# Kernel tuning notes

Measured on AMD Instinct MI355X. Metric: run time of the kernel, lower is better.

## Reference

```python
import jax, jax.numpy as jnp
import numpy as np

OUT_H, OUT_W = 64, 64  # glimpse size (layer's output_dim)
B, IMG_H, IMG_W, CH = 32, 512, 512, 3


def setup_inputs() -> dict:
    key = jax.random.key(0)
    k_img, k_u, k_s, k_d, k_u2, k_s2, k_d2 = jax.random.split(key, 7)
    img_tensor = jax.random.uniform(k_img, (B, IMG_H, IMG_W, CH), dtype=jnp.float32)
    # DRAW-style params per sample: (uy, sy, dy, ux, sx, dx)
    # centres u in [0, img - glimpse], sigma s in [1, 5], stride d in [1, img/glimpse]
    uy = jax.random.uniform(k_u, (B, 1), minval=0.0, maxval=IMG_H - OUT_H * 2.0)
    sy = jax.random.uniform(k_s, (B, 1), minval=1.0, maxval=5.0)
    dy = jax.random.uniform(k_d, (B, 1), minval=1.0, maxval=IMG_H / OUT_H)
    ux = jax.random.uniform(k_u2, (B, 1), minval=0.0, maxval=IMG_W - OUT_W * 2.0)
    sx = jax.random.uniform(k_s2, (B, 1), minval=1.0, maxval=5.0)
    dx = jax.random.uniform(k_d2, (B, 1), minval=1.0, maxval=IMG_W / OUT_W)
    transform_params = jnp.concatenate([uy, sy, dy, ux, sx, dx], axis=-1)  # (B, 6)
    return {"img_tensor": img_tensor, "transform_params": transform_params}


def gaussian_mask(u, s, d, R, C):
    """Normalized Gaussian filterbank.
    u, s, d: (B, 1) centre of first Gaussian, std, stride between centres.
    R: number of glimpse rows/cols; C: image size along that axis.
    Returns (B, C, R), each column normalized to sum 1 (plus eps)."""
    r = jnp.arange(R, dtype=jnp.float32).reshape(1, 1, R)
    c = jnp.arange(C, dtype=jnp.float32).reshape(1, C, 1)
    centres = u[:, None, :] + r * d[:, None, :]            # (B, 1, R)
    mask = jnp.exp(-0.5 * jnp.square((c - centres) / s[:, None, :]))  # (B, C, R)
    return mask / (jnp.sum(mask, axis=1, keepdims=True) + 1e-8)


def reference(img_tensor, transform_params):
    # img_tensor: (B, h, w, ch); transform_params: (B, 6)
    _, h, w, _ = img_tensor.shape
    uy, sy, dy, ux, sx, dx = jnp.split(transform_params, 6, axis=-1)
    Ay = gaussian_mask(uy, sy, dy, OUT_H, h)  # (B, h, OUT_H)
    Ax = gaussian_mask(ux, sx, dx, OUT_W, w)  # (B, w, OUT_W)
    # glimpse = Ay^T @ img @ Ax, applied per channel
    g = jnp.einsum('bhH,bhwc->bHwc', Ay, img_tensor)   # (B, OUT_H, w, ch)
    return jnp.einsum('bHwc,bwW->bHWc', g, Ax)         # (B, OUT_H, OUT_W, ch)
```

## Files before the change

kernel.cpp:

```cpp
#include <hip/hip_runtime.h>

#define BATCH 32
#define IMG 512
#define CH 3
#define GOUT 64
#define ROWB (IMG*CH)

typedef __attribute__((ext_vector_type(8))) short  short8;
typedef __attribute__((ext_vector_type(4))) float  floatx4;

__device__ __forceinline__ unsigned short f2bf(float x) {
    unsigned u = __builtin_bit_cast(unsigned, x);
    u += 0x7FFFu + ((u >> 16) & 1u);
    return (unsigned short)(u >> 16);
}

__global__ __launch_bounds__(64) void mask_kernel(const float* __restrict__ tp,
                                                  unsigned short* __restrict__ AyT,
                                                  unsigned short* __restrict__ AxT) {
    int blk  = blockIdx.x;
    int r    = blk & 63;
    int axis = (blk >> 6) & 1;
    int b    = blk >> 7;

    const float* p = tp + b*6 + (axis ? 3 : 0);
    float u = p[0], s = p[1], d = p[2];
    float centre = u + (float)r * d;
    float inv_s  = 1.0f / s;

    int lane = threadIdx.x;
    float e[8];
    float sum = 0.0f;
    #pragma unroll
    for (int i = 0; i < 8; ++i) {
        float z = ((float)(i*64 + lane) - centre) * inv_s;
        e[i] = __expf(-0.5f * z * z);
        sum += e[i];
    }
    #pragma unroll
    for (int m = 1; m < 64; m <<= 1)
        sum += __shfl_xor(sum, m, 64);
    float inv_sum = 1.0f / (sum + 1e-8f);

    unsigned short* dst = (axis ? AxT : AyT) + ((size_t)b*GOUT + r) * IMG;
    #pragma unroll
    for (int i = 0; i < 8; ++i)
        dst[i*64 + lane] = f2bf(e[i] * inv_sum);
}

__global__ __launch_bounds__(256) void stage1_kernel(const float* __restrict__ img,
                                                     const unsigned short* __restrict__ AyT,
                                                     float* __restrict__ gP) {
    int tile = blockIdx.x % 24;
    int b    = blockIdx.x / 24;
    int tid  = threadIdx.x;
    int wave = tid >> 6;
    int lane = tid & 63;
    int n16  = lane & 15;
    int q    = lane >> 4;
    int wc   = tile*64 + wave*16 + n16;

    floatx4 acc[4];
    #pragma unroll
    for (int mt = 0; mt < 4; ++mt) acc[mt] = (floatx4){0.f, 0.f, 0.f, 0.f};

    const unsigned short* ayb = AyT + ((size_t)b*GOUT + n16) * IMG;

    for (int h0 = 0; h0 < IMG; h0 += 32) {
        const float* bp = img + ((size_t)(b*IMG + h0 + q*8)) * ROWB + wc;
        short8 bf;
        #pragma unroll
        for (int j = 0; j < 8; ++j)
            bf[j] = (short)f2bf(bp[(size_t)j * ROWB]);

        #pragma unroll
        for (int mt = 0; mt < 4; ++mt) {
            short8 af = *(const short8*)(ayb + (size_t)mt*16*IMG + h0 + q*8);
            acc[mt] = __builtin_amdgcn_mfma_f32_16x16x32_bf16(af, bf, acc[mt], 0, 0, 0);
        }
    }

    int c = wc % 3, w = wc / 3;
    float* gb = gP + ((size_t)(b*CH + c) * GOUT) * IMG + w;
    #pragma unroll
    for (int mt = 0; mt < 4; ++mt) {
        int Hbase = mt*16 + q*4;
        #pragma unroll
        for (int reg = 0; reg < 4; ++reg)
            gb[(size_t)(Hbase + reg) * IMG] = acc[mt][reg];
    }
}

__global__ __launch_bounds__(256) void stage2_kernel(const float* __restrict__ gP,
                                                     const unsigned short* __restrict__ AxT,
                                                     float* __restrict__ out) {
    int blk  = blockIdx.x;
    int part = blk & 3;
    int bc   = blk >> 2;
    int c    = bc % 3;
    int b    = bc / 3;
    int tid  = threadIdx.x;
    int wm   = tid >> 6;
    int lane = tid & 63;
    int n16  = lane & 15;
    int q    = lane >> 4;

    floatx4 acc[4];
    #pragma unroll
    for (int nt = 0; nt < 4; ++nt) acc[nt] = (floatx4){0.f, 0.f, 0.f, 0.f};

    const float*          ga  = gP  + ((size_t)(b*CH + c) * GOUT + wm*16 + n16) * IMG;
    const unsigned short* axb = AxT + ((size_t)b*GOUT + n16) * IMG;

    #pragma unroll
    for (int cc = 0; cc < 4; ++cc) {
        int w0 = part*128 + cc*32;
        const float* ap = ga + w0 + q*8;
        short8 af;
        #pragma unroll
        for (int j = 0; j < 8; ++j)
            af[j] = (short)f2bf(ap[j]);

        #pragma unroll
        for (int nt = 0; nt < 4; ++nt) {
            short8 bf = *(const short8*)(axb + (size_t)nt*16*IMG + w0 + q*8);
            acc[nt] = __builtin_amdgcn_mfma_f32_16x16x32_bf16(af, bf, acc[nt], 0, 0, 0);
        }
    }

    #pragma unroll
    for (int nt = 0; nt < 4; ++nt) {
        int W = nt*16 + n16;
        #pragma unroll
        for (int reg = 0; reg < 4; ++reg) {
            int H = wm*16 + q*4 + reg;
            atomicAdd(out + (((size_t)b*GOUT + H) * GOUT + W) * CH + c, acc[nt][reg]);
        }
    }
}

extern "C" void kernel_launch(void* const* d_in, const int* in_sizes, int n_in,
                              void* d_out, int out_size, void* d_ws, size_t ws_size,
                              hipStream_t stream) {
    const float* img = (const float*)d_in[0];
    const float* tp  = (const float*)d_in[1];
    float* out = (float*)d_out;

    unsigned short* AyT = (unsigned short*)d_ws;
    unsigned short* AxT = AyT + (size_t)BATCH * GOUT * IMG;
    float*          gP  = (float*)(AxT + (size_t)BATCH * GOUT * IMG);

    hipMemsetAsync(d_out, 0, (size_t)out_size * sizeof(float), stream);
    mask_kernel  <<<BATCH * 2 * GOUT,  64, 0, stream>>>(tp, AyT, AxT);
    stage1_kernel<<<BATCH * 24,       256, 0, stream>>>(img, AyT, gP);
    stage2_kernel<<<BATCH * CH * 4,   256, 0, stream>>>(gP, AxT, out);
}
```

Measured before the change: 190.1 us.

## Stage image and mask tiles through LDS with vectorized loads in stage1

Stage1 now loads 64-row by 128-column image tiles and the matching Ay mask slice into shared memory using float4/uint4 loads, then feeds MFMAs from LDS. Each wave computes two N-tiles, and the grid is halved to 12 tiles per batch. The goal is to replace the strided scalar global loads with coalesced ones, at the cost of barriers, LDS footprint and fewer blocks. Stage2 also switches its A-fragment load to two float4 loads.

```diff
diff --git a/kernel.cpp b/kernel.cpp
--- a/kernel.cpp
+++ b/kernel.cpp
@@ -51,43 +51,78 @@
 __global__ __launch_bounds__(256) void stage1_kernel(const float* __restrict__ img,
                                                      const unsigned short* __restrict__ AyT,
                                                      float* __restrict__ gP) {
-    int tile = blockIdx.x % 24;
-    int b    = blockIdx.x / 24;
+    __shared__ float          Bs[64][132];
+    __shared__ unsigned short As[64][72];
+
+    int tile = blockIdx.x % 12;
+    int b    = blockIdx.x / 12;
+    int wc0  = tile * 128;
     int tid  = threadIdx.x;
     int wave = tid >> 6;
     int lane = tid & 63;
     int n16  = lane & 15;
     int q    = lane >> 4;
-    int wc   = tile*64 + wave*16 + n16;
 
-    floatx4 acc[4];
+    floatx4 acc[4][2];
     #pragma unroll
-    for (int mt = 0; mt < 4; ++mt) acc[mt] = (floatx4){0.f, 0.f, 0.f, 0.f};
+    for (int mt = 0; mt < 4; ++mt)
+        #pragma unroll
+        for (int nt = 0; nt < 2; ++nt)
+            acc[mt][nt] = (floatx4){0.f, 0.f, 0.f, 0.f};
 
-    const unsigned short* ayb = AyT + ((size_t)b*GOUT + n16) * IMG;
+    const float*          imb = img + (size_t)b * IMG * ROWB + wc0;
+    const unsigned short* ayb = AyT + (size_t)b * GOUT * IMG;
 
-    for (int h0 = 0; h0 < IMG; h0 += 32) {
-        const float* bp = img + ((size_t)(b*IMG + h0 + q*8)) * ROWB + wc;
-        short8 bf;
+    for (int h0 = 0; h0 < IMG; h0 += 64) {
         #pragma unroll
-        for (int j = 0; j < 8; ++j)
-            bf[j] = (short)f2bf(bp[(size_t)j * ROWB]);
+        for (int i = 0; i < 8; ++i) {
+            int p  = tid + i*256;
+            int r  = p >> 5;
+            int cg = p & 31;
+            float4 v = *(const float4*)(imb + (size_t)(h0 + r) * ROWB + cg*4);
+            *(float4*)&Bs[r][cg*4] = v;
+        }
+        #pragma unroll
+        for (int i = 0; i < 2; ++i) {
+            int p    = tid + i*256;
+            int r    = p >> 3;
+            int koff = (p & 7) * 8;
+            uint4 v = *(const uint4*)(ayb + (size_t)r * IMG + h0 + koff);
+            *(uint4*)&As[r][koff] = v;
+        }
+        __syncthreads();
 
         #pragma unroll
-        for (int mt = 0; mt < 4; ++mt) {
-            short8 af = *(const short8*)(ayb + (size_t)mt*16*IMG + h0 + q*8);
-            acc[mt] = __builtin_amdgcn_mfma_f32_16x16x32_bf16(af, bf, acc[mt], 0, 0, 0);
+        for (int s = 0; s < 2; ++s) {
+            short8 af[4];
+            #pragma unroll
+            for (int mt = 0; mt < 4; ++mt)
+                af[mt] = *(const short8*)&As[mt*16 + n16][s*32 + q*8];
+            #pragma unroll
+            for (int nt = 0; nt < 2; ++nt) {
+                short8 bf;
+                #pragma unroll
+                for (int j = 0; j < 8; ++j)
+                    bf[j] = (short)f2bf(Bs[s*32 + q*8 + j][wave*32 + nt*16 + n16]);
+                #pragma unroll
+                for (int mt = 0; mt < 4; ++mt)
+                    acc[mt][nt] = __builtin_amdgcn_mfma_f32_16x16x32_bf16(
+                        af[mt], bf, acc[mt][nt], 0, 0, 0);
+            }
         }
+        __syncthreads();
     }
 
-    int c = wc % 3, w = wc / 3;
-    float* gb = gP + ((size_t)(b*CH + c) * GOUT) * IMG + w;
     #pragma unroll
-    for (int mt = 0; mt < 4; ++mt) {
-        int Hbase = mt*16 + q*4;
+    for (int nt = 0; nt < 2; ++nt) {
+        int wc = wc0 + wave*32 + nt*16 + n16;
+        int c = wc % 3, w = wc / 3;
+        float* gb = gP + ((size_t)(b*CH + c) * GOUT) * IMG + w;
         #pragma unroll
-        for (int reg = 0; reg < 4; ++reg)
-            gb[(size_t)(Hbase + reg) * IMG] = acc[mt][reg];
+        for (int mt = 0; mt < 4; ++mt)
+            #pragma unroll
+            for (int reg = 0; reg < 4; ++reg)
+                gb[(size_t)(mt*16 + q*4 + reg) * IMG] = acc[mt][nt][reg];
     }
 }
 
@@ -116,10 +151,13 @@
     for (int cc = 0; cc < 4; ++cc) {
         int w0 = part*128 + cc*32;
         const float* ap = ga + w0 + q*8;
+        float4 a0 = *(const float4*)ap;
+        float4 a1 = *(const float4*)(ap + 4);
         short8 af;
-        #pragma unroll
-        for (int j = 0; j < 8; ++j)
-            af[j] = (short)f2bf(ap[j]);
+        af[0] = (short)f2bf(a0.x); af[1] = (short)f2bf(a0.y);
+        af[2] = (short)f2bf(a0.z); af[3] = (short)f2bf(a0.w);
+        af[4] = (short)f2bf(a1.x); af[5] = (short)f2bf(a1.y);
+        af[6] = (short)f2bf(a1.z); af[7] = (short)f2bf(a1.w);
 
         #pragma unroll
         for (int nt = 0; nt < 4; ++nt) {
@@ -152,6 +190,6 @@
 
     hipMemsetAsync(d_out, 0, (size_t)out_size * sizeof(float), stream);
     mask_kernel  <<<BATCH * 2 * GOUT,  64, 0, stream>>>(tp, AyT, AxT);
-    stage1_kernel<<<BATCH * 24,       256, 0, stream>>>(img, AyT, gP);
+    stage1_kernel<<<BATCH * 12,       256, 0, stream>>>(img, AyT, gP);
     stage2_kernel<<<BATCH * CH * 4,   256, 0, stream>>>(gP, AxT, out);
 }
```

Measured after the change: 199.8 us. +5.1%, slower.

## Stage image tiles in LDS via async loads and split stage-1 reduction over height

Applied to the files above, without the earlier changes.

Stage 1 now loads 64x64 fp32 image tiles into shared memory with direct global-to-LDS async loads and stages the Ay mask tile in LDS, in place of strided per-lane scalar global reads. The height reduction is split into two halves across twice as many blocks, each writing a separate partial buffer. Stage 2 sums the two partials with vectorized float4 loads before converting to bf16. The aim is better coalescing and more parallelism in the memory-bound first stage. In exchange it doubles the intermediate buffer traffic and workspace size and adds block-level syncs.

```diff
diff --git a/kernel.cpp b/kernel.cpp
--- a/kernel.cpp
+++ b/kernel.cpp
@@ -1,10 +1,12 @@
 #include <hip/hip_runtime.h>
+#include <stdint.h>
 
 #define BATCH 32
 #define IMG 512
 #define CH 3
 #define GOUT 64
 #define ROWB (IMG*CH)
+#define GP   ((size_t)BATCH*CH*GOUT*IMG)
 
 typedef __attribute__((ext_vector_type(8))) short  short8;
 typedef __attribute__((ext_vector_type(4))) float  floatx4;
@@ -13,6 +15,13 @@
     unsigned u = __builtin_bit_cast(unsigned, x);
     u += 0x7FFFu + ((u >> 16) & 1u);
     return (unsigned short)(u >> 16);
+}
+
+typedef __attribute__((address_space(3))) unsigned int  lds_u32;
+typedef __attribute__((address_space(1))) const unsigned int g_u32;
+__device__ __forceinline__ void async16(const void* g, void* l) {
+    __builtin_amdgcn_global_load_lds((g_u32*)(uintptr_t)g,
+                                     (lds_u32*)(uintptr_t)l, 16, 0, 0);
 }
 
 __global__ __launch_bounds__(64) void mask_kernel(const float* __restrict__ tp,
@@ -48,47 +57,75 @@
         dst[i*64 + lane] = f2bf(e[i] * inv_sum);
 }
 
-__global__ __launch_bounds__(256) void stage1_kernel(const float* __restrict__ img,
-                                                     const unsigned short* __restrict__ AyT,
-                                                     float* __restrict__ gP) {
-    int tile = blockIdx.x % 24;
-    int b    = blockIdx.x / 24;
+__global__ __launch_bounds__(256, 6) void stage1_kernel(const float* __restrict__ img,
+                                                        const unsigned short* __restrict__ AyT,
+                                                        float* __restrict__ gP) {
+    __shared__ float          Bs[64][64];
+    __shared__ unsigned short As[64][72];
+
+    int part = blockIdx.x & 1;
+    int bt   = blockIdx.x >> 1;
+    int tile = bt % 24;
+    int b    = bt / 24;
+    int wc0  = tile * 64;
     int tid  = threadIdx.x;
     int wave = tid >> 6;
     int lane = tid & 63;
     int n16  = lane & 15;
     int q    = lane >> 4;
-    int wc   = tile*64 + wave*16 + n16;
 
     floatx4 acc[4];
     #pragma unroll
     for (int mt = 0; mt < 4; ++mt) acc[mt] = (floatx4){0.f, 0.f, 0.f, 0.f};
 
-    const unsigned short* ayb = AyT + ((size_t)b*GOUT + n16) * IMG;
+    const float*          imb = img + (size_t)b * IMG * ROWB + wc0;
+    const unsigned short* ayb = AyT + (size_t)b * GOUT * IMG;
 
-    for (int h0 = 0; h0 < IMG; h0 += 32) {
-        const float* bp = img + ((size_t)(b*IMG + h0 + q*8)) * ROWB + wc;
-        short8 bf;
+    int rb = (tid >> 6)*4 + ((tid & 63) >> 4);
+    int cg = tid & 15;
+
+    for (int h0 = part*256; h0 < part*256 + 256; h0 += 64) {
+        uint4 av[2];
         #pragma unroll
-        for (int j = 0; j < 8; ++j)
-            bf[j] = (short)f2bf(bp[(size_t)j * ROWB]);
+        for (int i = 0; i < 2; ++i) {
+            int p = tid + i*256;
+            av[i] = *(const uint4*)(ayb + (size_t)(p >> 3) * IMG + h0 + (p & 7)*8);
+        }
+        #pragma unroll
+        for (int i = 0; i < 4; ++i) {
+            int r = rb + i*16;
+            async16(imb + (size_t)(h0 + r) * ROWB + cg*4, &Bs[r][cg*4]);
+        }
+        #pragma unroll
+        for (int i = 0; i < 2; ++i) {
+            int p = tid + i*256;
+            *(uint4*)&As[p >> 3][(p & 7)*8] = av[i];
+        }
+        __syncthreads();
 
         #pragma unroll
-        for (int mt = 0; mt < 4; ++mt) {
-            short8 af = *(const short8*)(ayb + (size_t)mt*16*IMG + h0 + q*8);
-            acc[mt] = __builtin_amdgcn_mfma_f32_16x16x32_bf16(af, bf, acc[mt], 0, 0, 0);
+        for (int s = 0; s < 2; ++s) {
+            short8 bf;
+            #pragma unroll
+            for (int j = 0; j < 8; ++j)
+                bf[j] = (short)f2bf(Bs[s*32 + q*8 + j][wave*16 + n16]);
+            #pragma unroll
+            for (int mt = 0; mt < 4; ++mt) {
+                short8 af = *(const short8*)&As[mt*16 + n16][s*32 + q*8];
+                acc[mt] = __builtin_amdgcn_mfma_f32_16x16x32_bf16(af, bf, acc[mt], 0, 0, 0);
+            }
         }
+        __syncthreads();
     }
 
+    int wc = wc0 + wave*16 + n16;
     int c = wc % 3, w = wc / 3;
-    float* gb = gP + ((size_t)(b*CH + c) * GOUT) * IMG + w;
+    float* gb = gP + (size_t)part * GP + ((size_t)(b*CH + c) * GOUT) * IMG + w;
     #pragma unroll
-    for (int mt = 0; mt < 4; ++mt) {
-        int Hbase = mt*16 + q*4;
+    for (int mt = 0; mt < 4; ++mt)
         #pragma unroll
         for (int reg = 0; reg < 4; ++reg)
-            gb[(size_t)(Hbase + reg) * IMG] = acc[mt][reg];
-    }
+            gb[(size_t)(mt*16 + q*4 + reg) * IMG] = acc[mt][reg];
 }
 
 __global__ __launch_bounds__(256) void stage2_kernel(const float* __restrict__ gP,
@@ -116,10 +153,15 @@
     for (int cc = 0; cc < 4; ++cc) {
         int w0 = part*128 + cc*32;
         const float* ap = ga + w0 + q*8;
+        float4 a0 = *(const float4*)ap;
+        float4 a1 = *(const float4*)(ap + 4);
+        float4 b0 = *(const float4*)(ap + GP);
+        float4 b1 = *(const float4*)(ap + GP + 4);
         short8 af;
-        #pragma unroll
-        for (int j = 0; j < 8; ++j)
-            af[j] = (short)f2bf(ap[j]);
+        af[0] = (short)f2bf(a0.x + b0.x); af[1] = (short)f2bf(a0.y + b0.y);
+        af[2] = (short)f2bf(a0.z + b0.z); af[3] = (short)f2bf(a0.w + b0.w);
+        af[4] = (short)f2bf(a1.x + b1.x); af[5] = (short)f2bf(a1.y + b1.y);
+        af[6] = (short)f2bf(a1.z + b1.z); af[7] = (short)f2bf(a1.w + b1.w);
 
         #pragma unroll
         for (int nt = 0; nt < 4; ++nt) {
@@ -148,10 +190,10 @@
 
     unsigned short* AyT = (unsigned short*)d_ws;
     unsigned short* AxT = AyT + (size_t)BATCH * GOUT * IMG;
-    float*          gP  = (float*)(AxT + (size_t)BATCH * GOUT * IMG);
+    float*          gPp = (float*)(AxT + (size_t)BATCH * GOUT * IMG);
 
     hipMemsetAsync(d_out, 0, (size_t)out_size * sizeof(float), stream);
-    mask_kernel  <<<BATCH * 2 * GOUT,  64, 0, stream>>>(tp, AyT, AxT);
-    stage1_kernel<<<BATCH * 24,       256, 0, stream>>>(img, AyT, gP);
-    stage2_kernel<<<BATCH * CH * 4,   256, 0, stream>>>(gP, AxT, out);
+    mask_kernel  <<<BATCH * 2 * GOUT,   64, 0, stream>>>(tp, AyT, AxT);
+    stage1_kernel<<<BATCH * 24 * 2,    256, 0, stream>>>(img, AyT, gPp);
+    stage2_kernel<<<BATCH * CH * 4,    256, 0, stream>>>(gPp, AxT, out);
 }
```

After: 185.9 us. 2.2% less time.

## Double-buffer image tiles via async global-to-LDS loads and store intermediate as bf16

Applied to the files above, without the earlier changes.

Stage 1 now streams image rows into LDS with asynchronous global_load_lds, double-buffered, and prefetches the next Ay fragments while the current MFMAs run. Blocks shrink to 128 threads with twice as many blocks. The intermediate is written as bf16 instead of fp32, which halves the intermediate traffic and lets stage 2 load fragments with single vector loads instead of converting per element. This adds an extra bf16 rounding of the intermediate, and correctness relies on the hand-written vmcnt waits matching the number of outstanding loads.

```diff
diff --git a/kernel.cpp b/kernel.cpp
--- a/kernel.cpp
+++ b/kernel.cpp
@@ -1,4 +1,5 @@
 #include <hip/hip_runtime.h>
+#include <stdint.h>
 
 #define BATCH 32
 #define IMG 512
@@ -13,6 +14,13 @@
     unsigned u = __builtin_bit_cast(unsigned, x);
     u += 0x7FFFu + ((u >> 16) & 1u);
     return (unsigned short)(u >> 16);
+}
+
+typedef __attribute__((address_space(3))) unsigned int  lds_u32;
+typedef __attribute__((address_space(1))) const unsigned int g_u32;
+__device__ __forceinline__ void async16(const void* g, void* l) {
+    __builtin_amdgcn_global_load_lds((g_u32*)(uintptr_t)g,
+                                     (lds_u32*)(uintptr_t)l, 16, 0, 0);
 }
 
 __global__ __launch_bounds__(64) void mask_kernel(const float* __restrict__ tp,
@@ -48,50 +56,79 @@
         dst[i*64 + lane] = f2bf(e[i] * inv_sum);
 }
 
-__global__ __launch_bounds__(256) void stage1_kernel(const float* __restrict__ img,
-                                                     const unsigned short* __restrict__ AyT,
-                                                     float* __restrict__ gP) {
-    int tile = blockIdx.x % 24;
-    int b    = blockIdx.x / 24;
+__global__ __launch_bounds__(128, 6) void stage1_kernel(const float* __restrict__ img,
+                                                        const unsigned short* __restrict__ AyT,
+                                                        unsigned short* __restrict__ gB) {
+    __shared__ float Bs[2][2][512];
+
+    int tile = blockIdx.x % 48;
+    int b    = blockIdx.x / 48;
     int tid  = threadIdx.x;
     int wave = tid >> 6;
     int lane = tid & 63;
     int n16  = lane & 15;
     int q    = lane >> 4;
-    int wc   = tile*64 + wave*16 + n16;
+    int wc0  = tile*32 + wave*16;
+
+    const float*          imb = img + (size_t)b*IMG*ROWB + wc0;
+    const unsigned short* ayb = AyT + ((size_t)b*GOUT + n16) * IMG;
+
+    int l4 = lane >> 2;
+    int c4 = (lane & 3) * 4;
+    int kb = (l4 >> 2) + 8*(l4 & 3);
 
     floatx4 acc[4];
     #pragma unroll
     for (int mt = 0; mt < 4; ++mt) acc[mt] = (floatx4){0.f, 0.f, 0.f, 0.f};
+    short8 af[2][4];
 
-    const unsigned short* ayb = AyT + ((size_t)b*GOUT + n16) * IMG;
+    #pragma unroll
+    for (int mt = 0; mt < 4; ++mt)
+        af[0][mt] = *(const short8*)(ayb + (size_t)mt*16*IMG + q*8);
+    #pragma unroll
+    for (int t = 0; t < 2; ++t)
+        async16(imb + (size_t)(kb + 4*t)*ROWB + c4, &Bs[wave][0][t*256 + lane*4]);
 
-    for (int h0 = 0; h0 < IMG; h0 += 32) {
-        const float* bp = img + ((size_t)(b*IMG + h0 + q*8)) * ROWB + wc;
+    #pragma unroll
+    for (int i = 0; i < 16; ++i) {
+        int buf = i & 1;
+        if (i < 15) {
+            int h1 = (i+1)*32;
+            #pragma unroll
+            for (int mt = 0; mt < 4; ++mt)
+                af[(i+1)&1][mt] = *(const short8*)(ayb + (size_t)mt*16*IMG + h1 + q*8);
+            #pragma unroll
+            for (int t = 0; t < 2; ++t)
+                async16(imb + (size_t)(h1 + kb + 4*t)*ROWB + c4,
+                        &Bs[wave][(i+1)&1][t*256 + lane*4]);
+            asm volatile("s_waitcnt vmcnt(6)" ::: "memory");
+        } else {
+            asm volatile("s_waitcnt vmcnt(0)" ::: "memory");
+        }
+        float tmp[8];
+        #pragma unroll
+        for (int j = 0; j < 8; ++j)
+            tmp[j] = Bs[wave][buf][(4*j + q)*16 + n16];
         short8 bf;
         #pragma unroll
         for (int j = 0; j < 8; ++j)
-            bf[j] = (short)f2bf(bp[(size_t)j * ROWB]);
-
+            bf[j] = (short)f2bf(tmp[j]);
         #pragma unroll
-        for (int mt = 0; mt < 4; ++mt) {
-            short8 af = *(const short8*)(ayb + (size_t)mt*16*IMG + h0 + q*8);
-            acc[mt] = __builtin_amdgcn_mfma_f32_16x16x32_bf16(af, bf, acc[mt], 0, 0, 0);
-        }
+        for (int mt = 0; mt < 4; ++mt)
+            acc[mt] = __builtin_amdgcn_mfma_f32_16x16x32_bf16(af[buf][mt], bf, acc[mt], 0, 0, 0);
     }
 
+    int wc = wc0 + n16;
     int c = wc % 3, w = wc / 3;
-    float* gb = gP + ((size_t)(b*CH + c) * GOUT) * IMG + w;
+    unsigned short* gb = gB + ((size_t)(b*CH + c) * GOUT) * IMG + w;
     #pragma unroll
-    for (int mt = 0; mt < 4; ++mt) {
-        int Hbase = mt*16 + q*4;
+    for (int mt = 0; mt < 4; ++mt)
         #pragma unroll
         for (int reg = 0; reg < 4; ++reg)
-            gb[(size_t)(Hbase + reg) * IMG] = acc[mt][reg];
-    }
+            gb[(size_t)(mt*16 + q*4 + reg) * IMG] = f2bf(acc[mt][reg]);
 }
 
-__global__ __launch_bounds__(256) void stage2_kernel(const float* __restrict__ gP,
+__global__ __launch_bounds__(256) void stage2_kernel(const unsigned short* __restrict__ gB,
                                                      const unsigned short* __restrict__ AxT,
                                                      float* __restrict__ out) {
     int blk  = blockIdx.x;
@@ -109,18 +146,13 @@
     #pragma unroll
     for (int nt = 0; nt < 4; ++nt) acc[nt] = (floatx4){0.f, 0.f, 0.f, 0.f};
 
-    const float*          ga  = gP  + ((size_t)(b*CH + c) * GOUT + wm*16 + n16) * IMG;
+    const unsigned short* ga  = gB  + ((size_t)(b*CH + c) * GOUT + wm*16 + n16) * IMG;
     const unsigned short* axb = AxT + ((size_t)b*GOUT + n16) * IMG;
 
     #pragma unroll
     for (int cc = 0; cc < 4; ++cc) {
         int w0 = part*128 + cc*32;
-        const float* ap = ga + w0 + q*8;
-        short8 af;
-        #pragma unroll
-        for (int j = 0; j < 8; ++j)
-            af[j] = (short)f2bf(ap[j]);
-
+        short8 af = *(const short8*)(ga + w0 + q*8);
         #pragma unroll
         for (int nt = 0; nt < 4; ++nt) {
             short8 bf = *(const short8*)(axb + (size_t)nt*16*IMG + w0 + q*8);
@@ -148,10 +180,10 @@
 
     unsigned short* AyT = (unsigned short*)d_ws;
     unsigned short* AxT = AyT + (size_t)BATCH * GOUT * IMG;
-    float*          gP  = (float*)(AxT + (size_t)BATCH * GOUT * IMG);
+    unsigned short* gB  = AxT + (size_t)BATCH * GOUT * IMG;
 
     hipMemsetAsync(d_out, 0, (size_t)out_size * sizeof(float), stream);
     mask_kernel  <<<BATCH * 2 * GOUT,  64, 0, stream>>>(tp, AyT, AxT);
-    stage1_kernel<<<BATCH * 24,       256, 0, stream>>>(img, AyT, gP);
-    stage2_kernel<<<BATCH * CH * 4,   256, 0, stream>>>(gP, AxT, out);
+    stage1_kernel<<<BATCH * 48,       128, 0, stream>>>(img, AyT, gB);
+    stage2_kernel<<<BATCH * CH * 4,   256, 0, stream>>>(gB, AxT, out);
 }
```

Result: slower. 197.9 us (+4.1%).
